# Performance work log

Hardware: AMD Instinct MI355X
Metric: run time of the kernel (lower is better)

Reference implementation:

```python
import jax, jax.numpy as jnp
import numpy as np

B, N, M, C, H = 2, 2048, 512, 1536, 12
HD = C // H          # 128 head dim
RD = 64              # partial rotary dim (rotary_dim in torch code)
EPS = 1e-6


def setup_inputs() -> dict:
    key = jax.random.key(0)
    ks = jax.random.split(key, 8)
    x = jax.random.normal(ks[0], (B, N, C), dtype=jnp.float32)
    y = jax.random.normal(ks[1], (B, M, C), dtype=jnp.float32)
    # realistic rope table: pos[n, j, 0]=cos, pos[n, j, 1]=sin, j over RD//2 freqs
    t = jnp.arange(N, dtype=jnp.float32)
    inv_freq = 1.0 / (10000.0 ** (jnp.arange(RD // 2, dtype=jnp.float32) / (RD // 2)))
    ang = t[:, None] * inv_freq[None, :]                     # [N, RD/2]
    pos = jnp.stack([jnp.cos(ang), jnp.sin(ang)], axis=-1)   # [N, RD/2, 2]
    y_token_weights = jax.random.uniform(ks[2], (B, M), dtype=jnp.float32, minval=0.05, maxval=2.0)
    s = 0.02
    Wqkv = jax.random.normal(ks[3], (C, 3 * C), dtype=jnp.float32) * s
    Wkv = jax.random.normal(ks[4], (C, 2 * C), dtype=jnp.float32) * s
    q_norm_w = jnp.ones((HD,), dtype=jnp.float32)
    k_norm_w = jnp.ones((HD,), dtype=jnp.float32)
    Wproj = jax.random.normal(ks[5], (C, C), dtype=jnp.float32) * s
    bproj = jnp.zeros((C,), dtype=jnp.float32)
    return {"x": x, "y": y, "pos": pos, "y_token_weights": y_token_weights,
            "Wqkv": Wqkv, "Wkv": Wkv, "q_norm_w": q_norm_w, "k_norm_w": k_norm_w,
            "Wproj": Wproj, "bproj": bproj}


def _rms_norm(h, w):
    # RMSNorm in fp32 then cast back (matches torch Norm)
    hf = h.astype(jnp.float32)
    var = jnp.mean(hf * hf, axis=-1, keepdims=True)
    return (w * (hf * jax.lax.rsqrt(var + EPS))).astype(h.dtype)


def _rope(q, k, pos):
    # q,k: [B,H,N,HD]; pos: [N, RD/2, 2]; rotate first RD dims only
    cos = pos[..., 0][None, None]            # [1,1,N,RD/2]
    sin = pos[..., 1][None, None]
    half = RD // 2

    def rot(t):
        t1 = t[..., :half]
        t2 = t[..., half:RD]
        t_rot = jnp.concatenate([t1 * cos - t2 * sin, t1 * sin + t2 * cos], axis=-1)
        return jnp.concatenate([t_rot, t[..., RD:]], axis=-1)

    return rot(q), rot(k)


def reference(x, y, pos, y_token_weights, Wqkv, Wkv, q_norm_w, k_norm_w, Wproj, bproj):
    # self QKV: [B,N,3C] -> [3,B,H,N,HD]
    qkv = jnp.einsum('bnc,cd->bnd', x, Wqkv).reshape(B, N, 3, H, HD).transpose(2, 0, 3, 1, 4)
    q, kx, vx = qkv[0], qkv[1], qkv[2]
    q = _rms_norm(q, q_norm_w)
    kx = _rms_norm(kx, k_norm_w)
    q, kx = _rope(q, kx, pos)

    # cross KV from y: [B,M,2C] -> [2,B,H,M,HD]
    kv = jnp.einsum('bmc,cd->bmd', y, Wkv).reshape(B, M, 2, H, HD).transpose(2, 0, 3, 1, 4)
    ky = _rms_norm(kv[0], k_norm_w)
    vy = kv[1]
    k = jnp.concatenate([kx, ky], axis=2)    # [B,H,N+M,HD]
    v = jnp.concatenate([vx, vy], axis=2)

    # additive bias: zeros over x tokens, log(clamp(w)) over y tokens
    y_bias = jnp.log(jnp.clip(y_token_weights, 1e-4, None))           # [B,M]
    attn_bias = jnp.concatenate([jnp.zeros((B, N), x.dtype), y_bias], axis=1)[:, None, None, :]

    scale = HD ** -0.5
    scores = jnp.einsum('bhnd,bhsd->bhns', q, k) * scale + attn_bias  # [B,H,N,N+M]
    attn = jax.nn.softmax(scores, axis=-1)
    out = jnp.einsum('bhns,bhsd->bhnd', attn, v)                      # [B,H,N,HD]
    out = out.transpose(0, 2, 1, 3).reshape(B, N, C)
    return jnp.einsum('bnc,cd->bnd', out, Wproj) + bproj
```

## Files before the change

### kernel.cpp

```cpp
#include <hip/hip_runtime.h>

typedef unsigned short u16;
typedef short bf16x8 __attribute__((ext_vector_type(8)));
typedef float f32x4 __attribute__((ext_vector_type(4)));
typedef u16 u16x4 __attribute__((ext_vector_type(4)));

#define DEVFN static __device__ __forceinline__

constexpr int Bz = 2, Nn = 2048, Mm = 512, Cc = 1536, Hh = 12, HD = 128;
constexpr int Ss = Nn + Mm;
constexpr float EPSV = 1e-6f;
constexpr float SCL = 0.08838834764831845f;

DEVFN u16 f2bf(float f) {
  union { float f; unsigned u; } v; v.f = f;
  unsigned r = v.u + 0x7fffu + ((v.u >> 16) & 1u);
  return (u16)(r >> 16);
}

DEVFN void gload16(const void* g, void* l) {
  __builtin_amdgcn_global_load_lds((const __attribute__((address_space(1))) void*)g,
                                   (__attribute__((address_space(3))) void*)l, 16, 0, 0);
}

DEVFN f32x4 mfma16(bf16x8 a, bf16x8 b, f32x4 c) {
  return __builtin_amdgcn_mfma_f32_16x16x32_bf16(a, b, c, 0, 0, 0);
}


__global__ void k_convert(const float* __restrict__ in, u16* __restrict__ out, int n) {
  int i = (blockIdx.x * blockDim.x + threadIdx.x) * 4;
  if (i < n) {
    float4 v = *(const float4*)(in + i);
    u16x4 o = { f2bf(v.x), f2bf(v.y), f2bf(v.z), f2bf(v.w) };
    *(u16x4*)(out + i) = o;
  }
}

__global__ void k_transpose_conv(const float* __restrict__ in, u16* __restrict__ out,
                                 int R, int Ccols) {
  __shared__ float t[32][33];
  int c0 = blockIdx.x * 32, r0 = blockIdx.y * 32;
  int lr = threadIdx.x >> 5, lc = threadIdx.x & 31;
#pragma unroll
  for (int i = 0; i < 4; ++i)
    t[lr + 8 * i][lc] = in[(long)(r0 + lr + 8 * i) * Ccols + c0 + lc];
  __syncthreads();
#pragma unroll
  for (int i = 0; i < 4; ++i)
    out[(long)(c0 + lr + 8 * i) * R + r0 + lc] = f2bf(t[lc][lr + 8 * i]);
}

__global__ void k_transpose_v(const u16* __restrict__ in, u16* __restrict__ out) {
  __shared__ u16 t[32][33];
  int bh = blockIdx.z;
  const u16* ib = in + (long)bh * Ss * HD;
  u16* ob = out + (long)bh * HD * Ss;
  int s0 = blockIdx.x * 32, d0 = blockIdx.y * 32;
  int lr = threadIdx.x >> 5, lc = threadIdx.x & 31;
#pragma unroll
  for (int i = 0; i < 4; ++i)
    t[lr + 8 * i][lc] = ib[(long)(s0 + lr + 8 * i) * HD + d0 + lc];
  __syncthreads();
#pragma unroll
  for (int i = 0; i < 4; ++i)
    ob[(long)(d0 + lr + 8 * i) * Ss + s0 + lc] = t[lc][lr + 8 * i];
}

__global__ void k_bias(const float* __restrict__ w, float* __restrict__ bias) {
  int i = blockIdx.x * 256 + threadIdx.x;
  if (i < Bz * Ss) {
    int b = i / Ss, s = i % Ss;
    bias[i] = (s < Nn) ? 0.0f : logf(fmaxf(w[b * Mm + s - Nn], 1e-4f));
  }
}

template <int MODE>
__global__ __launch_bounds__(256, 2) void k_gemm(
    const u16* __restrict__ A, const u16* __restrict__ Bt,
    int K, int NC, int rowsPerB,
    const float* __restrict__ pos, const float* __restrict__ qnw,
    const float* __restrict__ knw, const float* __restrict__ bprj,
    u16* __restrict__ qout, u16* __restrict__ kout, u16* __restrict__ vout,
    float* __restrict__ fout) {
  __shared__ __align__(16) u16 As[128 * 32];
  __shared__ __align__(16) u16 Bs[128 * 32];
  __shared__ float red[256];
  const int tid = threadIdx.x;
  const int lane = tid & 63;
  const int wid = tid >> 6;
  const int g = lane >> 4, cl = lane & 15;
  const int wr = wid >> 1, wc = wid & 1;
  const long m0 = (long)blockIdx.x * 128, n0 = (long)blockIdx.y * 128;

  f32x4 acc[4][4] = {};

  const int trA = tid >> 2;
  const int db = (tid & 3) ^ (trA & 3);
  const char* Ab = (const char*)A + (m0 + trA) * (long)K * 2 + db * 16;
  const char* Bb = (const char*)Bt + (n0 + trA) * (long)K * 2 + db * 16;
  const long rstep = (long)64 * K * 2;
  char* dstA0 = (char*)As + ((tid & ~63) << 4);
  char* dstB0 = (char*)Bs + ((tid & ~63) << 4);

  for (int kt = 0; kt < K / 32; ++kt) {
    __syncthreads();
    gload16(Ab + kt * 64, dstA0);
    gload16(Ab + kt * 64 + rstep, dstA0 + 4096);
    gload16(Bb + kt * 64, dstB0);
    gload16(Bb + kt * 64 + rstep, dstB0 + 4096);
    __syncthreads();
    bf16x8 af[4], bfr[4];
#pragma unroll
    for (int m = 0; m < 4; ++m) {
      int row = wr * 64 + m * 16 + cl;
      af[m] = *(const bf16x8*)((const char*)As + row * 64 + ((g ^ (row & 3)) << 4));
    }
#pragma unroll
    for (int n = 0; n < 4; ++n) {
      int row = wc * 64 + n * 16 + cl;
      bfr[n] = *(const bf16x8*)((const char*)Bs + row * 64 + ((g ^ (row & 3)) << 4));
    }
#pragma unroll
    for (int m = 0; m < 4; ++m)
#pragma unroll
      for (int n = 0; n < 4; ++n)
        acc[m][n] = mfma16(af[m], bfr[n], acc[m][n]);
  }

  if (MODE == 0) {
#pragma unroll
    for (int n = 0; n < 4; ++n) {
      int col = (int)n0 + wc * 64 + n * 16 + cl;
      float bv = bprj[col];
#pragma unroll
      for (int m = 0; m < 4; ++m)
#pragma unroll
        for (int r = 0; r < 4; ++r) {
          long row = m0 + wr * 64 + m * 16 + 4 * g + r;
          fout[row * NC + col] = acc[m][n][r] + bv;
        }
    }
    return;
  }

  const int ct = blockIdx.y;
  const int s_idx = ct / Hh, h = ct % Hh;
  const int bb = (int)(m0 / rowsPerB);
  const int bh = bb * Hh + h;
  const int seq0 = (int)(m0 % rowsPerB) + wr * 64;
  const bool do_norm = (MODE == 1) ? (s_idx < 2) : (s_idx == 0);
  const bool do_rope = (MODE == 1) && (s_idx < 2);

  if (do_norm) {
    float rs[4][4];
#pragma unroll
    for (int m = 0; m < 4; ++m)
#pragma unroll
      for (int r = 0; r < 4; ++r) {
        float t = 0.f;
#pragma unroll
        for (int n = 0; n < 4; ++n) t += acc[m][n][r] * acc[m][n][r];
        t += __shfl_xor(t, 1);
        t += __shfl_xor(t, 2);
        t += __shfl_xor(t, 4);
        t += __shfl_xor(t, 8);
        if (cl == 0) red[wc * 128 + wr * 64 + m * 16 + 4 * g + r] = t;
      }
    __syncthreads();
#pragma unroll
    for (int m = 0; m < 4; ++m)
#pragma unroll
      for (int r = 0; r < 4; ++r) {
        int row = wr * 64 + m * 16 + 4 * g + r;
        rs[m][r] = rsqrtf((red[row] + red[128 + row]) * (1.0f / 128.0f) + EPSV);
      }
    const float* nw = (MODE == 1 && s_idx == 0) ? qnw : knw;
#pragma unroll
    for (int n = 0; n < 4; ++n) {
      float nwv = nw[wc * 64 + n * 16 + cl];
#pragma unroll
      for (int m = 0; m < 4; ++m)
#pragma unroll
        for (int r = 0; r < 4; ++r) acc[m][n][r] *= rs[m][r] * nwv;
    }
  }

  if (do_rope && wc == 0) {
#pragma unroll
    for (int m = 0; m < 4; ++m)
#pragma unroll
      for (int r = 0; r < 4; ++r) {
        int seq = seq0 + m * 16 + 4 * g + r;
#pragma unroll
        for (int n = 0; n < 2; ++n) {
          int d = n * 16 + cl;
          float cs = pos[(seq * 32 + d) * 2 + 0];
          float sn = pos[(seq * 32 + d) * 2 + 1];
          float t1 = acc[m][n][r], t2 = acc[m][n + 2][r];
          acc[m][n][r] = t1 * cs - t2 * sn;
          acc[m][n + 2][r] = t1 * sn + t2 * cs;
        }
      }
  }

  u16* ob;
  long sbase;
  if (MODE == 1) {
    if (s_idx == 0) { ob = qout; sbase = (long)bh * Nn; }
    else if (s_idx == 1) { ob = kout; sbase = (long)bh * Ss; }
    else { ob = vout; sbase = (long)bh * Ss; }
  } else {
    ob = (s_idx == 0) ? kout : vout;
    sbase = (long)bh * Ss + Nn;
  }
#pragma unroll
  for (int m = 0; m < 4; ++m)
#pragma unroll
    for (int r = 0; r < 4; ++r) {
      long rowb = (sbase + seq0 + m * 16 + 4 * g + r) * HD;
#pragma unroll
      for (int n = 0; n < 4; ++n)
        ob[rowb + wc * 64 + n * 16 + cl] = f2bf(acc[m][n][r]);
    }
}

__global__ __launch_bounds__(256, 2) void k_flash(
    const u16* __restrict__ Q, const u16* __restrict__ K, const u16* __restrict__ Vt,
    const float* __restrict__ bias, u16* __restrict__ Aout) {
  __shared__ __align__(16) u16 Qs[128 * 128];
  __shared__ __align__(16) u16 Ks[64 * 128];
  __shared__ __align__(16) u16 Vs[128 * 64];
  __shared__ __align__(16) u16 Ps[4][32 * 64];
  const int tid = threadIdx.x;
  const int lane = tid & 63;
  const int wid = tid >> 6;
  const int g = lane >> 4, cl = lane & 15;
  const int bh = blockIdx.y, b = bh / Hh, h = bh % Hh;
  const int n0 = blockIdx.x * 128;

  const char* Qg = (const char*)(Q + ((long)bh * Nn + n0) * HD);
  const char* Kg = (const char*)(K + (long)bh * Ss * HD);
  const char* Vg = (const char*)(Vt + (long)bh * HD * Ss);
  const float* bg = bias + b * Ss;

  {
    int row = tid >> 4;
    int sw = ((tid & 15) ^ (row & 7)) << 4;
#pragma unroll
    for (int i = 0; i < 8; ++i)
      gload16(Qg + (row + i * 16) * 256 + sw, (char*)Qs + i * 4096 + ((tid & ~63) << 4));
  }
  const int krow_s = tid >> 4;
  const char* Ksrc0 = Kg + krow_s * 256 + (((tid & 15) ^ (krow_s & 7)) << 4);
  const int vrow_s = tid >> 3;
  const char* Vsrc0 = Vg + (long)vrow_s * (Ss * 2) + (((tid & 7) ^ (vrow_s & 7)) << 4);
  char* kd0 = (char*)Ks + ((tid & ~63) << 4);
  char* vd0 = (char*)Vs + ((tid & ~63) << 4);

#pragma unroll
  for (int i = 0; i < 4; ++i) gload16(Ksrc0 + i * 16 * 256, kd0 + i * 4096);
#pragma unroll
  for (int i = 0; i < 4; ++i) gload16(Vsrc0 + (long)i * 32 * (Ss * 2), vd0 + i * 4096);
  __syncthreads();

  bf16x8 qf[2][4];
#pragma unroll
  for (int m = 0; m < 2; ++m)
#pragma unroll
    for (int kk = 0; kk < 4; ++kk) {
      int row = wid * 32 + m * 16 + cl;
      qf[m][kk] = *(const bf16x8*)((const char*)Qs + row * 256 + (((kk * 4 + g) ^ (row & 7)) << 4));
    }

  f32x4 ov[2][8] = {};
  float mi[2][4], li[2][4];
#pragma unroll
  for (int m = 0; m < 2; ++m)
#pragma unroll
    for (int r = 0; r < 4; ++r) { mi[m][r] = -3.0e38f; li[m][r] = 0.f; }

  u16* pp = Ps[wid];

  for (int t = 0; t < Ss / 64; ++t) {
    const int kv0 = t * 64;
    f32x4 sc[2][4] = {};
#pragma unroll
    for (int n = 0; n < 4; ++n) {
      int krow = n * 16 + cl;
#pragma unroll
      for (int kk = 0; kk < 4; ++kk) {
        bf16x8 kf = *(const bf16x8*)((const char*)Ks + krow * 256 + (((kk * 4 + g) ^ (krow & 7)) << 4));
#pragma unroll
        for (int m = 0; m < 2; ++m) sc[m][n] = mfma16(qf[m][kk], kf, sc[m][n]);
      }
    }
    float bv[4];
#pragma unroll
    for (int n = 0; n < 4; ++n) bv[n] = bg[kv0 + n * 16 + cl];
    float corr[2][4];
#pragma unroll
    for (int m = 0; m < 2; ++m)
#pragma unroll
      for (int r = 0; r < 4; ++r) {
        float mx = -3.0e38f;
#pragma unroll
        for (int n = 0; n < 4; ++n) {
          float s = sc[m][n][r] * SCL + bv[n];
          sc[m][n][r] = s;
          mx = fmaxf(mx, s);
        }
        mx = fmaxf(mx, __shfl_xor(mx, 1));
        mx = fmaxf(mx, __shfl_xor(mx, 2));
        mx = fmaxf(mx, __shfl_xor(mx, 4));
        mx = fmaxf(mx, __shfl_xor(mx, 8));
        float mnew = fmaxf(mi[m][r], mx);
        float co = __expf(mi[m][r] - mnew);
        mi[m][r] = mnew;
        float rsum = 0.f;
#pragma unroll
        for (int n = 0; n < 4; ++n) {
          float p = __expf(sc[m][n][r] - mnew);
          sc[m][n][r] = p;
          rsum += p;
        }
        rsum += __shfl_xor(rsum, 1);
        rsum += __shfl_xor(rsum, 2);
        rsum += __shfl_xor(rsum, 4);
        rsum += __shfl_xor(rsum, 8);
        li[m][r] = li[m][r] * co + rsum;
        corr[m][r] = co;
      }
#pragma unroll
    for (int m = 0; m < 2; ++m)
#pragma unroll
      for (int nd = 0; nd < 8; ++nd)
#pragma unroll
        for (int r = 0; r < 4; ++r) ov[m][nd][r] *= corr[m][r];

#pragma unroll
    for (int m = 0; m < 2; ++m)
#pragma unroll
      for (int n = 0; n < 4; ++n)
#pragma unroll
        for (int r = 0; r < 4; ++r) {
          int prow = m * 16 + 4 * g + r, col = n * 16 + cl;
          pp[prow * 64 + (((col >> 3) ^ (prow & 7)) << 3) + (col & 7)] = f2bf(sc[m][n][r]);
        }
    bf16x8 pf[2][2];
#pragma unroll
    for (int m = 0; m < 2; ++m)
#pragma unroll
      for (int ks = 0; ks < 2; ++ks) {
        int row = m * 16 + cl;
        pf[m][ks] = *(const bf16x8*)((const char*)pp + row * 128 + (((ks * 4 + g) ^ (row & 7)) << 4));
      }
#pragma unroll
    for (int nd = 0; nd < 8; ++nd) {
      int vrow = nd * 16 + cl;
#pragma unroll
      for (int ks = 0; ks < 2; ++ks) {
        bf16x8 vf = *(const bf16x8*)((const char*)Vs + vrow * 128 + (((ks * 4 + g) ^ (vrow & 7)) << 4));
#pragma unroll
        for (int m = 0; m < 2; ++m) ov[m][nd] = mfma16(pf[m][ks], vf, ov[m][nd]);
      }
    }
    if (t + 1 < Ss / 64) {
      __syncthreads();
      const long kn = (long)(t + 1) * 64;
#pragma unroll
      for (int i = 0; i < 4; ++i) gload16(Ksrc0 + kn * 256 + i * 16 * 256, kd0 + i * 4096);
#pragma unroll
      for (int i = 0; i < 4; ++i) gload16(Vsrc0 + kn * 2 + (long)i * 32 * (Ss * 2), vd0 + i * 4096);
      __syncthreads();
    }
  }

#pragma unroll
  for (int m = 0; m < 2; ++m)
#pragma unroll
    for (int r = 0; r < 4; ++r) {
      float inv = 1.0f / li[m][r];
      long row = (long)b * Nn + n0 + wid * 32 + m * 16 + 4 * g + r;
      long base = row * Cc + h * HD;
#pragma unroll
      for (int nd = 0; nd < 8; ++nd)
        Aout[base + nd * 16 + cl] = f2bf(ov[m][nd][r] * inv);
    }
}


extern "C" void kernel_launch(void* const* d_in, const int* in_sizes, int n_in,
                              void* d_out, int out_size, void* d_ws, size_t ws_size,
                              hipStream_t stream) {
  const float* x = (const float*)d_in[0];
  const float* y = (const float*)d_in[1];
  const float* pos = (const float*)d_in[2];
  const float* ytw = (const float*)d_in[3];
  const float* Wqkv = (const float*)d_in[4];
  const float* Wkv = (const float*)d_in[5];
  const float* qnw = (const float*)d_in[6];
  const float* knw = (const float*)d_in[7];
  const float* Wproj = (const float*)d_in[8];
  const float* bproj = (const float*)d_in[9];
  float* out = (float*)d_out;
  char* ws = (char*)d_ws;

  size_t o = 0;
  auto take = [&](size_t b) {
    char* p = ws + o;
    o += (b + 255) & ~(size_t)255;
    return p;
  };
  u16* xb = (u16*)take((size_t)Bz * Nn * Cc * 2);
  u16* yb = (u16*)take((size_t)Bz * Mm * Cc * 2);
  u16* wqkvt = (u16*)take((size_t)3 * Cc * Cc * 2);
  u16* wkvt = (u16*)take((size_t)2 * Cc * Cc * 2);
  u16* wprjt = (u16*)take((size_t)Cc * Cc * 2);
  u16* qb = (u16*)take((size_t)Bz * Hh * Nn * HD * 2);
  u16* kb = (u16*)take((size_t)Bz * Hh * Ss * HD * 2);
  u16* vb = (u16*)take((size_t)Bz * Hh * Ss * HD * 2);
  u16* vtb = (u16*)take((size_t)Bz * Hh * Ss * HD * 2);
  u16* ab = (u16*)take((size_t)Bz * Nn * Cc * 2);
  float* bias = (float*)take((size_t)Bz * Ss * 4);

  k_convert<<<dim3(Bz * Nn * Cc / 1024), 256, 0, stream>>>(x, xb, Bz * Nn * Cc);
  k_convert<<<dim3(Bz * Mm * Cc / 1024), 256, 0, stream>>>(y, yb, Bz * Mm * Cc);
  k_transpose_conv<<<dim3(3 * Cc / 32, Cc / 32), 256, 0, stream>>>(Wqkv, wqkvt, Cc, 3 * Cc);
  k_transpose_conv<<<dim3(2 * Cc / 32, Cc / 32), 256, 0, stream>>>(Wkv, wkvt, Cc, 2 * Cc);
  k_transpose_conv<<<dim3(Cc / 32, Cc / 32), 256, 0, stream>>>(Wproj, wprjt, Cc, Cc);
  k_bias<<<dim3((Bz * Ss + 255) / 256), 256, 0, stream>>>(ytw, bias);
  k_gemm<1><<<dim3(Bz * Nn / 128, 3 * Cc / 128), 256, 0, stream>>>(
      xb, wqkvt, Cc, 3 * Cc, Nn, pos, qnw, knw, nullptr, qb, kb, vb, nullptr);
  k_gemm<2><<<dim3(Bz * Mm / 128, 2 * Cc / 128), 256, 0, stream>>>(
      yb, wkvt, Cc, 2 * Cc, Mm, pos, qnw, knw, nullptr, nullptr, kb, vb, nullptr);
  k_transpose_v<<<dim3(Ss / 32, HD / 32, Bz * Hh), 256, 0, stream>>>(vb, vtb);
  k_flash<<<dim3(Nn / 128, Bz * Hh), 256, 0, stream>>>(qb, kb, vtb, bias, ab);
  k_gemm<0><<<dim3(Bz * Nn / 128, Cc / 128), 256, 0, stream>>>(
      ab, wprjt, Cc, Cc, Nn, nullptr, nullptr, nullptr, bproj, nullptr, nullptr, nullptr, out);
}
```

Baseline: 472.8 us.

## Load K/V fragments directly from global in flash kernel, shrink query tile

The flash-attention kernel stops staging Q, K and V in LDS and instead loads MFMA fragments straight from global memory. Each wave now handles 16 query rows instead of 32, the block tile drops from 128 to 64 queries, and launch bounds request 3 blocks per CU. This removes the barriers and LDS traffic around K/V staging and raises occupancy. In exchange each wave re-reads K/V from global/L2 with no sharing inside the block, so total K/V traffic roughly quadruples and the kernel may become memory-bound.

```diff
diff --git a/kernel.cpp b/kernel.cpp
--- a/kernel.cpp
+++ b/kernel.cpp
@@ -225,168 +225,119 @@
     }
 }
 
-__global__ __launch_bounds__(256, 2) void k_flash(
+constexpr int PSTR = 72;
+
+__global__ __launch_bounds__(256, 3) void k_flash(
     const u16* __restrict__ Q, const u16* __restrict__ K, const u16* __restrict__ Vt,
     const float* __restrict__ bias, u16* __restrict__ Aout) {
-  __shared__ __align__(16) u16 Qs[128 * 128];
-  __shared__ __align__(16) u16 Ks[64 * 128];
-  __shared__ __align__(16) u16 Vs[128 * 64];
-  __shared__ __align__(16) u16 Ps[4][32 * 64];
+  __shared__ __align__(16) u16 Ps[4][16 * PSTR];
   const int tid = threadIdx.x;
   const int lane = tid & 63;
   const int wid = tid >> 6;
   const int g = lane >> 4, cl = lane & 15;
   const int bh = blockIdx.y, b = bh / Hh, h = bh % Hh;
-  const int n0 = blockIdx.x * 128;
-
-  const char* Qg = (const char*)(Q + ((long)bh * Nn + n0) * HD);
-  const char* Kg = (const char*)(K + (long)bh * Ss * HD);
-  const char* Vg = (const char*)(Vt + (long)bh * HD * Ss);
+  const int n0 = blockIdx.x * 64;
+
+  const u16* Qg = Q + ((long)bh * Nn + n0 + wid * 16) * HD;
+  const u16* Kg = K + (long)bh * Ss * HD;
+  const u16* Vg = Vt + (long)bh * HD * Ss;
   const float* bg = bias + b * Ss;
 
-  {
-    int row = tid >> 4;
-    int sw = ((tid & 15) ^ (row & 7)) << 4;
-#pragma unroll
-    for (int i = 0; i < 8; ++i)
-      gload16(Qg + (row + i * 16) * 256 + sw, (char*)Qs + i * 4096 + ((tid & ~63) << 4));
-  }
-  const int krow_s = tid >> 4;
-  const char* Ksrc0 = Kg + krow_s * 256 + (((tid & 15) ^ (krow_s & 7)) << 4);
-  const int vrow_s = tid >> 3;
-  const char* Vsrc0 = Vg + (long)vrow_s * (Ss * 2) + (((tid & 7) ^ (vrow_s & 7)) << 4);
-  char* kd0 = (char*)Ks + ((tid & ~63) << 4);
-  char* vd0 = (char*)Vs + ((tid & ~63) << 4);
-
-#pragma unroll
-  for (int i = 0; i < 4; ++i) gload16(Ksrc0 + i * 16 * 256, kd0 + i * 4096);
-#pragma unroll
-  for (int i = 0; i < 4; ++i) gload16(Vsrc0 + (long)i * 32 * (Ss * 2), vd0 + i * 4096);
-  __syncthreads();
-
-  bf16x8 qf[2][4];
-#pragma unroll
-  for (int m = 0; m < 2; ++m)
-#pragma unroll
-    for (int kk = 0; kk < 4; ++kk) {
-      int row = wid * 32 + m * 16 + cl;
-      qf[m][kk] = *(const bf16x8*)((const char*)Qs + row * 256 + (((kk * 4 + g) ^ (row & 7)) << 4));
-    }
-
-  f32x4 ov[2][8] = {};
-  float mi[2][4], li[2][4];
-#pragma unroll
-  for (int m = 0; m < 2; ++m)
-#pragma unroll
-    for (int r = 0; r < 4; ++r) { mi[m][r] = -3.0e38f; li[m][r] = 0.f; }
+  bf16x8 qf[4];
+#pragma unroll
+  for (int kk = 0; kk < 4; ++kk)
+    qf[kk] = *(const bf16x8*)(Qg + cl * HD + kk * 32 + g * 8);
+
+  f32x4 ov[8] = {};
+  float mi[4], li[4];
+#pragma unroll
+  for (int r = 0; r < 4; ++r) { mi[r] = -3.0e38f; li[r] = 0.f; }
 
   u16* pp = Ps[wid];
 
   for (int t = 0; t < Ss / 64; ++t) {
     const int kv0 = t * 64;
-    f32x4 sc[2][4] = {};
+    f32x4 sc[4] = {};
 #pragma unroll
     for (int n = 0; n < 4; ++n) {
-      int krow = n * 16 + cl;
+      const u16* kr = Kg + (long)(kv0 + n * 16 + cl) * HD + g * 8;
 #pragma unroll
       for (int kk = 0; kk < 4; ++kk) {
-        bf16x8 kf = *(const bf16x8*)((const char*)Ks + krow * 256 + (((kk * 4 + g) ^ (krow & 7)) << 4));
-#pragma unroll
-        for (int m = 0; m < 2; ++m) sc[m][n] = mfma16(qf[m][kk], kf, sc[m][n]);
+        bf16x8 kf = *(const bf16x8*)(kr + kk * 32);
+        sc[n] = mfma16(qf[kk], kf, sc[n]);
       }
     }
     float bv[4];
 #pragma unroll
     for (int n = 0; n < 4; ++n) bv[n] = bg[kv0 + n * 16 + cl];
-    float corr[2][4];
-#pragma unroll
-    for (int m = 0; m < 2; ++m)
+    float corr[4];
+#pragma unroll
+    for (int r = 0; r < 4; ++r) {
+      float mx = -3.0e38f;
+#pragma unroll
+      for (int n = 0; n < 4; ++n) {
+        float s = sc[n][r] * SCL + bv[n];
+        sc[n][r] = s;
+        mx = fmaxf(mx, s);
+      }
+      mx = fmaxf(mx, __shfl_xor(mx, 1));
+      mx = fmaxf(mx, __shfl_xor(mx, 2));
+      mx = fmaxf(mx, __shfl_xor(mx, 4));
+      mx = fmaxf(mx, __shfl_xor(mx, 8));
+      float mnew = fmaxf(mi[r], mx);
+      float co = __expf(mi[r] - mnew);
+      mi[r] = mnew;
+      float rsum = 0.f;
+#pragma unroll
+      for (int n = 0; n < 4; ++n) {
+        float p = __expf(sc[n][r] - mnew);
+        sc[n][r] = p;
+        rsum += p;
+      }
+      rsum += __shfl_xor(rsum, 1);
+      rsum += __shfl_xor(rsum, 2);
+      rsum += __shfl_xor(rsum, 4);
+      rsum += __shfl_xor(rsum, 8);
+      li[r] = li[r] * co + rsum;
+      corr[r] = co;
+    }
+#pragma unroll
+    for (int nd = 0; nd < 8; ++nd)
+#pragma unroll
+      for (int r = 0; r < 4; ++r) ov[nd][r] *= corr[r];
+
+#pragma unroll
+    for (int n = 0; n < 4; ++n)
 #pragma unroll
       for (int r = 0; r < 4; ++r) {
-        float mx = -3.0e38f;
-#pragma unroll
-        for (int n = 0; n < 4; ++n) {
-          float s = sc[m][n][r] * SCL + bv[n];
-          sc[m][n][r] = s;
-          mx = fmaxf(mx, s);
-        }
-        mx = fmaxf(mx, __shfl_xor(mx, 1));
-        mx = fmaxf(mx, __shfl_xor(mx, 2));
-        mx = fmaxf(mx, __shfl_xor(mx, 4));
-        mx = fmaxf(mx, __shfl_xor(mx, 8));
-        float mnew = fmaxf(mi[m][r], mx);
-        float co = __expf(mi[m][r] - mnew);
-        mi[m][r] = mnew;
-        float rsum = 0.f;
-#pragma unroll
-        for (int n = 0; n < 4; ++n) {
-          float p = __expf(sc[m][n][r] - mnew);
-          sc[m][n][r] = p;
-          rsum += p;
-        }
-        rsum += __shfl_xor(rsum, 1);
-        rsum += __shfl_xor(rsum, 2);
-        rsum += __shfl_xor(rsum, 4);
-        rsum += __shfl_xor(rsum, 8);
-        li[m][r] = li[m][r] * co + rsum;
-        corr[m][r] = co;
-      }
-#pragma unroll
-    for (int m = 0; m < 2; ++m)
-#pragma unroll
-      for (int nd = 0; nd < 8; ++nd)
-#pragma unroll
-        for (int r = 0; r < 4; ++r) ov[m][nd][r] *= corr[m][r];
-
-#pragma unroll
-    for (int m = 0; m < 2; ++m)
-#pragma unroll
-      for (int n = 0; n < 4; ++n)
-#pragma unroll
-        for (int r = 0; r < 4; ++r) {
-          int prow = m * 16 + 4 * g + r, col = n * 16 + cl;
-          pp[prow * 64 + (((col >> 3) ^ (prow & 7)) << 3) + (col & 7)] = f2bf(sc[m][n][r]);
-        }
-    bf16x8 pf[2][2];
-#pragma unroll
-    for (int m = 0; m < 2; ++m)
+        int prow = 4 * g + r, col = n * 16 + cl;
+        pp[prow * PSTR + (((col >> 3) ^ (prow & 7)) << 3) + (col & 7)] = f2bf(sc[n][r]);
+      }
+    bf16x8 pf[2];
+#pragma unroll
+    for (int ks = 0; ks < 2; ++ks)
+      pf[ks] = *(const bf16x8*)((const char*)pp + cl * (PSTR * 2) +
+                                (((ks * 4 + g) ^ (cl & 7)) << 4));
+#pragma unroll
+    for (int nd = 0; nd < 8; ++nd) {
+      const u16* vr = Vg + (long)(nd * 16 + cl) * Ss + kv0 + g * 8;
 #pragma unroll
       for (int ks = 0; ks < 2; ++ks) {
-        int row = m * 16 + cl;
-        pf[m][ks] = *(const bf16x8*)((const char*)pp + row * 128 + (((ks * 4 + g) ^ (row & 7)) << 4));
-      }
-#pragma unroll
-    for (int nd = 0; nd < 8; ++nd) {
-      int vrow = nd * 16 + cl;
-#pragma unroll
-      for (int ks = 0; ks < 2; ++ks) {
-        bf16x8 vf = *(const bf16x8*)((const char*)Vs + vrow * 128 + (((ks * 4 + g) ^ (vrow & 7)) << 4));
-#pragma unroll
-        for (int m = 0; m < 2; ++m) ov[m][nd] = mfma16(pf[m][ks], vf, ov[m][nd]);
-      }
-    }
-    if (t + 1 < Ss / 64) {
-      __syncthreads();
-      const long kn = (long)(t + 1) * 64;
-#pragma unroll
-      for (int i = 0; i < 4; ++i) gload16(Ksrc0 + kn * 256 + i * 16 * 256, kd0 + i * 4096);
-#pragma unroll
-      for (int i = 0; i < 4; ++i) gload16(Vsrc0 + kn * 2 + (long)i * 32 * (Ss * 2), vd0 + i * 4096);
-      __syncthreads();
-    }
-  }
-
-#pragma unroll
-  for (int m = 0; m < 2; ++m)
-#pragma unroll
-    for (int r = 0; r < 4; ++r) {
-      float inv = 1.0f / li[m][r];
-      long row = (long)b * Nn + n0 + wid * 32 + m * 16 + 4 * g + r;
-      long base = row * Cc + h * HD;
-#pragma unroll
-      for (int nd = 0; nd < 8; ++nd)
-        Aout[base + nd * 16 + cl] = f2bf(ov[m][nd][r] * inv);
-    }
+        bf16x8 vf = *(const bf16x8*)(vr + ks * 32);
+        ov[nd] = mfma16(pf[ks], vf, ov[nd]);
+      }
+    }
+  }
+
+#pragma unroll
+  for (int r = 0; r < 4; ++r) {
+    float inv = 1.0f / li[r];
+    long row = (long)b * Nn + n0 + wid * 16 + 4 * g + r;
+    long base = row * Cc + h * HD;
+#pragma unroll
+    for (int nd = 0; nd < 8; ++nd)
+      Aout[base + nd * 16 + cl] = f2bf(ov[nd][r] * inv);
+  }
 }
 
 
@@ -435,7 +386,7 @@
   k_gemm<2><<<dim3(Bz * Mm / 128, 2 * Cc / 128), 256, 0, stream>>>(
       yb, wkvt, Cc, 2 * Cc, Mm, pos, qnw, knw, nullptr, nullptr, kb, vb, nullptr);
   k_transpose_v<<<dim3(Ss / 32, HD / 32, Bz * Hh), 256, 0, stream>>>(vb, vtb);
-  k_flash<<<dim3(Nn / 128, Bz * Hh), 256, 0, stream>>>(qb, kb, vtb, bias, ab);
+  k_flash<<<dim3(Nn / 64, Bz * Hh), 256, 0, stream>>>(qb, kb, vtb, bias, ab);
   k_gemm<0><<<dim3(Bz * Nn / 128, Cc / 128), 256, 0, stream>>>(
       ab, wprjt, Cc, Cc, Nn, nullptr, nullptr, nullptr, bproj, nullptr, nullptr, nullptr, out);
 }
```

Result: slower. 764.2 us (+61.6%).

## Double-buffer K/V in flash attention and compute transposed scores

Applied to the files above, without the earlier changes.

Restructures the flash attention kernel. K/V tiles go into two shared-memory buffers so the next tile is prefetched while the current one is computed, which leaves one barrier per iteration instead of two. Scores are computed as K·Q^T so each lane holds one query row's values, reducing softmax reductions to two cross-group shuffles. The softmax scale is folded into the Q norm weights and the bias add is skipped for the x-token range. Q fragments load straight from global memory, dropping the Q shared-memory stage, and P is packed with v_cvt_pk_bf16_f32. This adds LDS and register pressure, which could reduce occupancy.

```diff
diff --git a/kernel.cpp b/kernel.cpp
--- a/kernel.cpp
+++ b/kernel.cpp
@@ -16,6 +16,12 @@
   union { float f; unsigned u; } v; v.f = f;
   unsigned r = v.u + 0x7fffu + ((v.u >> 16) & 1u);
   return (u16)(r >> 16);
+}
+
+DEVFN unsigned cvtpk(float lo, float hi) {
+  unsigned r;
+  asm("v_cvt_pk_bf16_f32 %0, %1, %2" : "=v"(r) : "v"(lo), "v"(hi));
+  return r;
 }
 
 DEVFN void gload16(const void* g, void* l) {
@@ -176,9 +182,10 @@
         rs[m][r] = rsqrtf((red[row] + red[128 + row]) * (1.0f / 128.0f) + EPSV);
       }
     const float* nw = (MODE == 1 && s_idx == 0) ? qnw : knw;
+    const float nsc = (MODE == 1 && s_idx == 0) ? SCL : 1.0f;
 #pragma unroll
     for (int n = 0; n < 4; ++n) {
-      float nwv = nw[wc * 64 + n * 16 + cl];
+      float nwv = nw[wc * 64 + n * 16 + cl] * nsc;
 #pragma unroll
       for (int m = 0; m < 4; ++m)
 #pragma unroll
@@ -228,165 +235,162 @@
 __global__ __launch_bounds__(256, 2) void k_flash(
     const u16* __restrict__ Q, const u16* __restrict__ K, const u16* __restrict__ Vt,
     const float* __restrict__ bias, u16* __restrict__ Aout) {
-  __shared__ __align__(16) u16 Qs[128 * 128];
-  __shared__ __align__(16) u16 Ks[64 * 128];
-  __shared__ __align__(16) u16 Vs[128 * 64];
-  __shared__ __align__(16) u16 Ps[4][32 * 64];
-  const int tid = threadIdx.x;
-  const int lane = tid & 63;
-  const int wid = tid >> 6;
+  __shared__ __align__(16) u16 Ks[2][64 * 128];
+  __shared__ __align__(16) u16 Vs[2][128 * 64];
+  __shared__ __align__(16) u16 Ps[4][16 * 64];
+  const int tid = threadIdx.x, lane = tid & 63, wid = tid >> 6;
   const int g = lane >> 4, cl = lane & 15;
   const int bh = blockIdx.y, b = bh / Hh, h = bh % Hh;
   const int n0 = blockIdx.x * 128;
-
-  const char* Qg = (const char*)(Q + ((long)bh * Nn + n0) * HD);
+  constexpr int NT = Ss / 64;
+
+  const u16* Qg = Q + ((long)bh * Nn + n0 + wid * 32) * HD;
   const char* Kg = (const char*)(K + (long)bh * Ss * HD);
   const char* Vg = (const char*)(Vt + (long)bh * HD * Ss);
   const float* bg = bias + b * Ss;
 
-  {
-    int row = tid >> 4;
-    int sw = ((tid & 15) ^ (row & 7)) << 4;
-#pragma unroll
-    for (int i = 0; i < 8; ++i)
-      gload16(Qg + (row + i * 16) * 256 + sw, (char*)Qs + i * 4096 + ((tid & ~63) << 4));
-  }
-  const int krow_s = tid >> 4;
-  const char* Ksrc0 = Kg + krow_s * 256 + (((tid & 15) ^ (krow_s & 7)) << 4);
-  const int vrow_s = tid >> 3;
-  const char* Vsrc0 = Vg + (long)vrow_s * (Ss * 2) + (((tid & 7) ^ (vrow_s & 7)) << 4);
-  char* kd0 = (char*)Ks + ((tid & ~63) << 4);
-  char* vd0 = (char*)Vs + ((tid & ~63) << 4);
-
-#pragma unroll
-  for (int i = 0; i < 4; ++i) gload16(Ksrc0 + i * 16 * 256, kd0 + i * 4096);
-#pragma unroll
-  for (int i = 0; i < 4; ++i) gload16(Vsrc0 + (long)i * 32 * (Ss * 2), vd0 + i * 4096);
+  bf16x8 qf[2][4];
+#pragma unroll
+  for (int m = 0; m < 2; ++m)
+#pragma unroll
+    for (int kk = 0; kk < 4; ++kk)
+      qf[m][kk] = *(const bf16x8*)(Qg + (m * 16 + cl) * HD + kk * 32 + g * 8);
+
+  const int krow = tid >> 4;
+  const char* Ksrc = Kg + krow * 256 + (((tid & 15) ^ (krow & 7)) << 4);
+  const int vrow = tid >> 3;
+  const char* Vsrc = Vg + (long)vrow * (Ss * 2) + (((tid & 7) ^ (vrow & 7)) << 4);
+  const int dsto = (tid & ~63) << 4;
+
+  auto STAGE = [&](int t, int s) {
+    char* kd = (char*)Ks[s] + dsto;
+    char* vd = (char*)Vs[s] + dsto;
+    long kb = (long)t * 64;
+#pragma unroll
+    for (int i = 0; i < 4; ++i) gload16(Ksrc + kb * 256 + i * (16 * 256), kd + i * 4096);
+#pragma unroll
+    for (int i = 0; i < 4; ++i) gload16(Vsrc + kb * 2 + (long)i * 32 * (Ss * 2), vd + i * 4096);
+  };
+
+  f32x4 ov[2][8] = {};
+  float mi[2] = {-3e38f, -3e38f}, li[2] = {0.f, 0.f};
+  u16* pt = (u16*)Ps[wid];
+  const int h7 = (cl & 7) << 1;
+
+  STAGE(0, 0);
   __syncthreads();
-
-  bf16x8 qf[2][4];
-#pragma unroll
-  for (int m = 0; m < 2; ++m)
-#pragma unroll
-    for (int kk = 0; kk < 4; ++kk) {
-      int row = wid * 32 + m * 16 + cl;
-      qf[m][kk] = *(const bf16x8*)((const char*)Qs + row * 256 + (((kk * 4 + g) ^ (row & 7)) << 4));
-    }
-
-  f32x4 ov[2][8] = {};
-  float mi[2][4], li[2][4];
-#pragma unroll
-  for (int m = 0; m < 2; ++m)
-#pragma unroll
-    for (int r = 0; r < 4; ++r) { mi[m][r] = -3.0e38f; li[m][r] = 0.f; }
-
-  u16* pp = Ps[wid];
-
-  for (int t = 0; t < Ss / 64; ++t) {
-    const int kv0 = t * 64;
+  int cur = 0;
+  for (int t = 0; t < NT; ++t) {
+    if (t + 1 < NT) STAGE(t + 1, cur ^ 1);
+    const bool biased = (t * 64 >= Nn);
+    float badd[4][4];
+    if (biased) {
+#pragma unroll
+      for (int n = 0; n < 4; ++n)
+#pragma unroll
+        for (int r = 0; r < 4; ++r)
+          badd[n][r] = bg[t * 64 + n * 16 + 4 * g + r];
+    }
+    const char* ks = (const char*)Ks[cur];
+    const char* vs = (const char*)Vs[cur];
+
     f32x4 sc[2][4] = {};
 #pragma unroll
     for (int n = 0; n < 4; ++n) {
-      int krow = n * 16 + cl;
+      int krw = n * 16 + cl;
 #pragma unroll
       for (int kk = 0; kk < 4; ++kk) {
-        bf16x8 kf = *(const bf16x8*)((const char*)Ks + krow * 256 + (((kk * 4 + g) ^ (krow & 7)) << 4));
-#pragma unroll
-        for (int m = 0; m < 2; ++m) sc[m][n] = mfma16(qf[m][kk], kf, sc[m][n]);
-      }
-    }
-    float bv[4];
-#pragma unroll
-    for (int n = 0; n < 4; ++n) bv[n] = bg[kv0 + n * 16 + cl];
-    float corr[2][4];
-#pragma unroll
-    for (int m = 0; m < 2; ++m)
-#pragma unroll
-      for (int r = 0; r < 4; ++r) {
-        float mx = -3.0e38f;
-#pragma unroll
-        for (int n = 0; n < 4; ++n) {
-          float s = sc[m][n][r] * SCL + bv[n];
+        bf16x8 kf = *(const bf16x8*)(ks + krw * 256 + (((kk * 4 + g) ^ (krw & 7)) << 4));
+        sc[0][n] = mfma16(kf, qf[0][kk], sc[0][n]);
+        sc[1][n] = mfma16(kf, qf[1][kk], sc[1][n]);
+      }
+    }
+
+    float co_s[2];
+#pragma unroll
+    for (int m = 0; m < 2; ++m) {
+      float mx = -3e38f;
+#pragma unroll
+      for (int n = 0; n < 4; ++n)
+#pragma unroll
+        for (int r = 0; r < 4; ++r) {
+          float s = sc[m][n][r];
+          if (biased) s += badd[n][r];
           sc[m][n][r] = s;
           mx = fmaxf(mx, s);
         }
-        mx = fmaxf(mx, __shfl_xor(mx, 1));
-        mx = fmaxf(mx, __shfl_xor(mx, 2));
-        mx = fmaxf(mx, __shfl_xor(mx, 4));
-        mx = fmaxf(mx, __shfl_xor(mx, 8));
-        float mnew = fmaxf(mi[m][r], mx);
-        float co = __expf(mi[m][r] - mnew);
-        mi[m][r] = mnew;
-        float rsum = 0.f;
-#pragma unroll
-        for (int n = 0; n < 4; ++n) {
+      mx = fmaxf(mx, __shfl_xor(mx, 16));
+      mx = fmaxf(mx, __shfl_xor(mx, 32));
+      float mnew = fmaxf(mi[m], mx);
+      float co = __expf(mi[m] - mnew);
+      mi[m] = mnew;
+      float rsum = 0.f;
+#pragma unroll
+      for (int n = 0; n < 4; ++n)
+#pragma unroll
+        for (int r = 0; r < 4; ++r) {
           float p = __expf(sc[m][n][r] - mnew);
           sc[m][n][r] = p;
           rsum += p;
         }
-        rsum += __shfl_xor(rsum, 1);
-        rsum += __shfl_xor(rsum, 2);
-        rsum += __shfl_xor(rsum, 4);
-        rsum += __shfl_xor(rsum, 8);
-        li[m][r] = li[m][r] * co + rsum;
-        corr[m][r] = co;
-      }
+      rsum += __shfl_xor(rsum, 16);
+      rsum += __shfl_xor(rsum, 32);
+      li[m] = li[m] * co + rsum;
+      co_s[m] = co;
+    }
+
 #pragma unroll
     for (int m = 0; m < 2; ++m)
 #pragma unroll
-      for (int nd = 0; nd < 8; ++nd)
-#pragma unroll
-        for (int r = 0; r < 4; ++r) ov[m][nd][r] *= corr[m][r];
-
-#pragma unroll
-    for (int m = 0; m < 2; ++m)
-#pragma unroll
-      for (int n = 0; n < 4; ++n)
-#pragma unroll
-        for (int r = 0; r < 4; ++r) {
-          int prow = m * 16 + 4 * g + r, col = n * 16 + cl;
-          pp[prow * 64 + (((col >> 3) ^ (prow & 7)) << 3) + (col & 7)] = f2bf(sc[m][n][r]);
-        }
+      for (int r = 0; r < 4; ++r) {
+        float cr = __shfl(co_s[m], 4 * g + r, 64);
+#pragma unroll
+        for (int nd = 0; nd < 8; ++nd) ov[m][nd][r] *= cr;
+      }
+
     bf16x8 pf[2][2];
 #pragma unroll
-    for (int m = 0; m < 2; ++m)
-#pragma unroll
-      for (int ks = 0; ks < 2; ++ks) {
-        int row = m * 16 + cl;
-        pf[m][ks] = *(const bf16x8*)((const char*)pp + row * 128 + (((ks * 4 + g) ^ (row & 7)) << 4));
-      }
+    for (int m = 0; m < 2; ++m) {
+#pragma unroll
+      for (int n = 0; n < 4; ++n) {
+        uint2 w;
+        w.x = cvtpk(sc[m][n][0], sc[m][n][1]);
+        w.y = cvtpk(sc[m][n][2], sc[m][n][3]);
+        *(uint2*)((char*)pt + cl * 128 + (((4 * n + g) ^ h7) << 3)) = w;
+      }
+#pragma unroll
+      for (int ks2 = 0; ks2 < 2; ++ks2)
+        pf[m][ks2] = *(const bf16x8*)((const char*)pt + cl * 128 +
+                                      (((8 * ks2 + 2 * g) ^ h7) << 3));
+    }
+
 #pragma unroll
     for (int nd = 0; nd < 8; ++nd) {
-      int vrow = nd * 16 + cl;
-#pragma unroll
-      for (int ks = 0; ks < 2; ++ks) {
-        bf16x8 vf = *(const bf16x8*)((const char*)Vs + vrow * 128 + (((ks * 4 + g) ^ (vrow & 7)) << 4));
-#pragma unroll
-        for (int m = 0; m < 2; ++m) ov[m][nd] = mfma16(pf[m][ks], vf, ov[m][nd]);
-      }
-    }
-    if (t + 1 < Ss / 64) {
-      __syncthreads();
-      const long kn = (long)(t + 1) * 64;
-#pragma unroll
-      for (int i = 0; i < 4; ++i) gload16(Ksrc0 + kn * 256 + i * 16 * 256, kd0 + i * 4096);
-#pragma unroll
-      for (int i = 0; i < 4; ++i) gload16(Vsrc0 + kn * 2 + (long)i * 32 * (Ss * 2), vd0 + i * 4096);
-      __syncthreads();
-    }
-  }
-
-#pragma unroll
-  for (int m = 0; m < 2; ++m)
+      int vrw = nd * 16 + cl;
+#pragma unroll
+      for (int ks2 = 0; ks2 < 2; ++ks2) {
+        bf16x8 vf = *(const bf16x8*)(vs + vrw * 128 + (((ks2 * 4 + g) ^ (vrw & 7)) << 4));
+        ov[0][nd] = mfma16(pf[0][ks2], vf, ov[0][nd]);
+        ov[1][nd] = mfma16(pf[1][ks2], vf, ov[1][nd]);
+      }
+    }
+    __syncthreads();
+    cur ^= 1;
+  }
+
+#pragma unroll
+  for (int m = 0; m < 2; ++m) {
+    float inv = 1.0f / li[m];
 #pragma unroll
     for (int r = 0; r < 4; ++r) {
-      float inv = 1.0f / li[m][r];
+      float iv = __shfl(inv, 4 * g + r, 64);
       long row = (long)b * Nn + n0 + wid * 32 + m * 16 + 4 * g + r;
       long base = row * Cc + h * HD;
 #pragma unroll
       for (int nd = 0; nd < 8; ++nd)
-        Aout[base + nd * 16 + cl] = f2bf(ov[m][nd][r] * inv);
-    }
+        Aout[base + nd * 16 + cl] = f2bf(ov[m][nd][r] * iv);
+    }
+  }
 }
 
 
```

New measurement: 427.4 us. -9.6%, faster.
